# Optimization experiments

Hardware: AMD Instinct MI355X
Metric: run time of the kernel (lower is better)

The kernel has to match this reference:

```python
import jax, jax.numpy as jnp
import numpy as np

# ---- static config (Phi-3-small layer 0, blocksparse branch) ----
HIDDEN = 4096
N_HEADS = 32
N_KV = 8
HEAD_DIM = HIDDEN // N_HEADS        # 128
Q_PER_KV = N_HEADS // N_KV          # 4
SEQ = 2048
ROPE_BASE = 1000000.0
POS_SCALE = 1.0
SM_SCALE = 1.0 / HEAD_DIM           # mup scaling, multiplier=1.0
BLOCK = 64
LOCAL_BLOCKS = 16
VERT_STRIDE = 8


def _blocksparse_mask(seq_len):
    """Dense [S,S] bool mask realizing the causal blocksparse pattern:
    query block i attends key block j iff j<=i and (i-j < LOCAL_BLOCKS or (j+1) % VERT_STRIDE == 0),
    with elementwise causality inside blocks. Built once in numpy (static)."""
    nb = seq_len // BLOCK
    qb = np.arange(nb)[:, None]
    kb = np.arange(nb)[None, :]
    bmask = (kb <= qb) & ((qb - kb < LOCAL_BLOCKS) | ((kb + 1) % VERT_STRIDE == 0))
    emask = np.kron(bmask, np.ones((BLOCK, BLOCK), dtype=bool))
    i = np.arange(seq_len)
    emask &= i[:, None] >= i[None, :]
    return jnp.asarray(emask)


def _rope(x, cos, sin):
    # x: [B, S, H, D]; cos/sin: [S, D]
    x1, x2 = jnp.split(x, 2, axis=-1)
    rot = jnp.concatenate([-x2, x1], axis=-1)
    return x * cos[None, :, None, :] + rot * sin[None, :, None, :]


def setup_inputs() -> dict:
    key = jax.random.key(0)
    k1, k2, k3, k4, k5 = jax.random.split(key, 5)
    qkv_out = (N_HEADS + 2 * N_KV) * HEAD_DIM  # 6144
    return {
        "hidden_states": jax.random.normal(k1, (1, SEQ, HIDDEN), dtype=jnp.float32),
        "w_qkv": jax.random.normal(k2, (qkv_out, HIDDEN), dtype=jnp.float32) * 0.02,
        "b_qkv": jnp.zeros((qkv_out,), dtype=jnp.float32),
        "w_dense": jax.random.normal(k3, (HIDDEN, HIDDEN), dtype=jnp.float32) * 0.02,
        "b_dense": jnp.zeros((HIDDEN,), dtype=jnp.float32),
    }


def reference(hidden_states, w_qkv, b_qkv, w_dense, b_dense):
    B, S, _ = hidden_states.shape
    # grouped QKV projection: [B,S,(H+2*KV)*D]
    qkv = jnp.einsum("bsh,oh->bso", hidden_states, w_qkv) + b_qkv
    # group layout: (group, q0..q3, k, v) per kv head
    qkv = qkv.reshape(B, S, N_KV, Q_PER_KV + 2, HEAD_DIM)
    q = qkv[:, :, :, :Q_PER_KV].reshape(B, S, N_HEADS, HEAD_DIM)
    k = qkv[:, :, :, Q_PER_KV]   # [B,S,KV,D]
    v = qkv[:, :, :, Q_PER_KV + 1]
    # rotary embeddings (HF rotate-half style)
    inv_freq = 1.0 / (ROPE_BASE ** (jnp.arange(0, HEAD_DIM, 2, dtype=jnp.float32) / HEAD_DIM))
    t = jnp.arange(S, dtype=jnp.float32) * POS_SCALE
    freqs = jnp.outer(t, inv_freq)               # [S, D/2]
    emb = jnp.concatenate([freqs, freqs], axis=-1)
    cos, sin = jnp.cos(emb), jnp.sin(emb)
    q = _rope(q, cos, sin)
    k = _rope(k, cos, sin)
    # GQA: replicate kv heads to match q heads
    k = jnp.repeat(k, Q_PER_KV, axis=2)          # [B,S,H,D]
    v = jnp.repeat(v, Q_PER_KV, axis=2)
    mask = _blocksparse_mask(S)                  # [S,S] bool
    scores = jnp.einsum("bqhd,bkhd->bhqk", q, k) * SM_SCALE
    scores = jnp.where(mask[None, None], scores, jnp.finfo(scores.dtype).min)
    probs = jax.nn.softmax(scores, axis=-1)
    ctx = jnp.einsum("bhqk,bkhd->bqhd", probs, v).reshape(B, S, HIDDEN)
    out = jnp.einsum("bsh,oh->bso", ctx, w_dense) + b_dense
    return out
```

## Files before the change

kernel.cpp:

```cpp
#include <hip/hip_runtime.h>
#include <hip/hip_bf16.h>

#define SEQ 2048
#define HIDDEN 4096
#define NH 32
#define NKV 8
#define HD 128
#define QKV_OUT 6144
#define QSCALE (0.0078125f * 1.4426950408889634f)

typedef __attribute__((ext_vector_type(8))) short bf16x8;
typedef __attribute__((ext_vector_type(4))) float f32x4;
typedef __attribute__((ext_vector_type(16))) float f32x16;

__device__ inline unsigned short f32_bf16(float f) {
  union { float f; unsigned int u; } v; v.f = f;
  unsigned int r = v.u + 0x7FFFu + ((v.u >> 16) & 1u);
  return (unsigned short)(r >> 16);
}
__device__ inline float bf16_f32(unsigned short u) {
  union { unsigned int u; float f; } v; v.u = (unsigned int)u << 16;
  return v.f;
}
__device__ inline unsigned int pk(float a, float b) {
  union { __hip_bfloat162 h; unsigned int u; } t;
  t.h = __float22bfloat162_rn(make_float2(a, b));
  return t.u;
}
__device__ inline void pswap(unsigned int &a, unsigned int &b) {
  auto r = __builtin_amdgcn_permlane32_swap((int)a, (int)b, false, false);
  a = (unsigned int)r[0]; b = (unsigned int)r[1];
}
__device__ inline float xmax32(float v) {
  int x = __builtin_bit_cast(int, v);
  auto r = __builtin_amdgcn_permlane32_swap(x, x, false, false);
  return fmaxf(__builtin_bit_cast(float, (int)r[0]), __builtin_bit_cast(float, (int)r[1]));
}
__device__ inline float xadd32(float v) {
  int x = __builtin_bit_cast(int, v);
  auto r = __builtin_amdgcn_permlane32_swap(x, x, false, false);
  return __builtin_bit_cast(float, (int)r[0]) + __builtin_bit_cast(float, (int)r[1]);
}

__device__ inline void cast8(const float* __restrict__ in, unsigned short* __restrict__ out) {
  float4 a = *reinterpret_cast<const float4*>(in);
  float4 b = *reinterpret_cast<const float4*>(in + 4);
  unsigned short t[8];
  t[0] = f32_bf16(a.x); t[1] = f32_bf16(a.y); t[2] = f32_bf16(a.z); t[3] = f32_bf16(a.w);
  t[4] = f32_bf16(b.x); t[5] = f32_bf16(b.y); t[6] = f32_bf16(b.z); t[7] = f32_bf16(b.w);
  *reinterpret_cast<uint4*>(out) = *reinterpret_cast<uint4*>(t);
}

#define N1 ((size_t)SEQ * HIDDEN / 8)
#define N2 ((size_t)QKV_OUT * HIDDEN / 8)
#define N3 ((size_t)SEQ * 64)
__global__ __launch_bounds__(256) void prep(const float* __restrict__ hid,
                                            unsigned short* __restrict__ hid_bf,
                                            const float* __restrict__ wq,
                                            unsigned short* __restrict__ wq_bf,
                                            float* __restrict__ ct,
                                            float* __restrict__ st) {
  size_t i = (size_t)blockIdx.x * 256 + threadIdx.x;
  if (i < N1) {
    cast8(hid + i * 8, hid_bf + i * 8);
  } else if (i < N1 + N2) {
    size_t j = (i - N1) * 8;
    cast8(wq + j, wq_bf + j);
  } else {
    size_t j = i - N1 - N2;
    int s = (int)(j >> 6), d = (int)(j & 63);
    float inv = powf(1.0e6f, -(float)d * (1.0f / 64.0f));
    float f = (float)s * inv;
    ct[j] = cosf(f);
    st[j] = sinf(f);
  }
}

template <int BM, int CR, int CC, bool OBF, bool FC>
__global__ __launch_bounds__(512, 2) void gemm9(const unsigned short* __restrict__ A,
                                                const unsigned short* __restrict__ B,
                                                const float* __restrict__ bias,
                                                void* __restrict__ Cp,
                                                int M, int N, int K,
                                                const float* __restrict__ cw_in,
                                                unsigned short* __restrict__ cw_out,
                                                size_t cw_n, int ngemm) {
  constexpr int BN = 256;
  constexpr int MQ = BM / 64;
  constexpr int La = BM / 128;
  constexpr int Lb = 2;
  constexpr int AH = BM * 64;
  constexpr int BUF = AH * 2 + 32768;
  __shared__ __align__(16) char Lds[BUF * 2];

  if constexpr (FC) {
    if ((int)blockIdx.x >= ngemm) {
      size_t base = ((size_t)(blockIdx.x - ngemm) * 512 + threadIdx.x) * 8;
      size_t stride = (size_t)(gridDim.x - ngemm) * 512 * 8;
      for (size_t i = base; i < cw_n; i += stride)
        cast8(cw_in + i, cw_out + i);
      return;
    }
  }

  const int tid = threadIdx.x;
  const int wave = tid >> 6, lane = tid & 63;
  const int wr = wave >> 2, wc = wave & 3;
  const int lrow = lane & 15, lgrp = lane >> 4;

  const int ntx = N / BN;
  const int wg0 = blockIdx.x;
  const int xcd = wg0 & 7, w = wg0 >> 3;
  const int cpb = ntx / CC;
  const int band = xcd / cpb, colc = xcd % cpb;
  const int bm = (band * CR + w / CC) * BM;
  const int bn = (colc * CC + w % CC) * BN;

  const int srow8 = lane >> 3;
  const int scol = ((lane & 7) ^ srow8) * 8;
  const unsigned short* gsrc[2 * La + 2 * Lb];
  int ldsoff[2 * La + 2 * Lb];
#pragma unroll
  for (int u = 0; u < 2; ++u)
#pragma unroll
    for (int j = 0; j < La; ++j) {
      int row = bm + u * (BM / 2) + (wave * La + j) * 8 + srow8;
      gsrc[u * La + j] = A + (size_t)row * K + scol;
      ldsoff[u * La + j] = u * AH + (wave * La + j) * 1024;
    }
#pragma unroll
  for (int u = 0; u < 2; ++u)
#pragma unroll
    for (int j = 0; j < Lb; ++j) {
      int row = bn + u * 128 + (wave * Lb + j) * 8 + srow8;
      gsrc[2 * La + u * Lb + j] = B + (size_t)row * K + scol;
      ldsoff[2 * La + u * Lb + j] = 2 * AH + u * 16384 + (wave * Lb + j) * 1024;
    }

  auto stage = [&](int bufb, int u, int k0) {
    const int lo = (u < 2) ? u * La : 2 * La + (u - 2) * Lb;
    const int nl = (u < 2) ? La : Lb;
#pragma unroll
    for (int j = 0; j < 4; ++j)
      if (j < nl)
        __builtin_amdgcn_global_load_lds(
            (const __attribute__((address_space(1))) unsigned int*)(gsrc[lo + j] + k0),
            (__attribute__((address_space(3))) unsigned int*)(Lds + bufb + ldsoff[lo + j]),
            16, 0, 0);
  };

  const int rsw = (lrow & 7) << 4;
  auto aoff = [&](int mh, int m, int ks) {
    int r = mh * (BM / 4) + m * 16 + lrow;
    return wr * AH + r * 128 + ((ks * 64 + lgrp * 16) ^ rsw);
  };
  auto boff = [&](int nh, int n, int ks) {
    int r = (wc & 1) * 64 + nh * 32 + n * 16 + lrow;
    return 2 * AH + (wc >> 1) * 16384 + r * 128 + ((ks * 64 + lgrp * 16) ^ rsw);
  };

  f32x4 acc[2 * MQ][4] = {};
  bf16x8 af[MQ][2], bf0[2][2], bf1[2][2];

  const int nt = K / 64;
#pragma unroll
  for (int u = 0; u < 4; ++u) stage(0, u, 0);

  for (int t = 0; t < nt; ++t) {
    const int cur = (t & 1) ? BUF : 0;
    const int nxt = cur ^ BUF;
    const bool pf = (t + 1) < nt;
    const int k1 = (t + 1) * 64;
    const char* base = Lds + cur;

    if (pf) stage(nxt, 0, k1);
    if (pf) { if constexpr (La == 2) asm volatile("s_waitcnt vmcnt(2)" ::: "memory");
              else                   asm volatile("s_waitcnt vmcnt(1)" ::: "memory"); }
    else      asm volatile("s_waitcnt vmcnt(0)" ::: "memory");
    __builtin_amdgcn_sched_barrier(0);
    __builtin_amdgcn_s_barrier();
    __builtin_amdgcn_sched_barrier(0);
#pragma unroll
    for (int m = 0; m < MQ; ++m)
#pragma unroll
      for (int ks = 0; ks < 2; ++ks)
        af[m][ks] = *reinterpret_cast<const bf16x8*>(base + aoff(0, m, ks));
#pragma unroll
    for (int n = 0; n < 2; ++n)
#pragma unroll
      for (int ks = 0; ks < 2; ++ks)
        bf0[n][ks] = *reinterpret_cast<const bf16x8*>(base + boff(0, n, ks));
    __builtin_amdgcn_s_setprio(1);
#pragma unroll
    for (int m = 0; m < MQ; ++m)
#pragma unroll
      for (int n = 0; n < 2; ++n)
#pragma unroll
        for (int ks = 0; ks < 2; ++ks)
          acc[m][n] = __builtin_amdgcn_mfma_f32_16x16x32_bf16(af[m][ks], bf0[n][ks], acc[m][n], 0, 0, 0);
    __builtin_amdgcn_s_setprio(0);

    if (pf) stage(nxt, 1, k1);
#pragma unroll
    for (int n = 0; n < 2; ++n)
#pragma unroll
      for (int ks = 0; ks < 2; ++ks)
        bf1[n][ks] = *reinterpret_cast<const bf16x8*>(base + boff(1, n, ks));
    __builtin_amdgcn_s_setprio(1);
#pragma unroll
    for (int m = 0; m < MQ; ++m)
#pragma unroll
      for (int n = 0; n < 2; ++n)
#pragma unroll
        for (int ks = 0; ks < 2; ++ks)
          acc[m][2 + n] = __builtin_amdgcn_mfma_f32_16x16x32_bf16(af[m][ks], bf1[n][ks], acc[m][2 + n], 0, 0, 0);
    __builtin_amdgcn_s_setprio(0);

    if (pf) stage(nxt, 2, k1);
#pragma unroll
    for (int m = 0; m < MQ; ++m)
#pragma unroll
      for (int ks = 0; ks < 2; ++ks)
        af[m][ks] = *reinterpret_cast<const bf16x8*>(base + aoff(1, m, ks));
    __builtin_amdgcn_s_setprio(1);
#pragma unroll
    for (int m = 0; m < MQ; ++m)
#pragma unroll
      for (int n = 0; n < 2; ++n)
#pragma unroll
        for (int ks = 0; ks < 2; ++ks)
          acc[MQ + m][n] = __builtin_amdgcn_mfma_f32_16x16x32_bf16(af[m][ks], bf0[n][ks], acc[MQ + m][n], 0, 0, 0);
    __builtin_amdgcn_s_setprio(0);

    if (pf) stage(nxt, 3, k1);
    __builtin_amdgcn_s_setprio(1);
#pragma unroll
    for (int m = 0; m < MQ; ++m)
#pragma unroll
      for (int n = 0; n < 2; ++n)
#pragma unroll
        for (int ks = 0; ks < 2; ++ks)
          acc[MQ + m][2 + n] = __builtin_amdgcn_mfma_f32_16x16x32_bf16(af[m][ks], bf1[n][ks], acc[MQ + m][2 + n], 0, 0, 0);
    __builtin_amdgcn_s_setprio(0);
  }

#pragma unroll
  for (int ni = 0; ni < 4; ++ni) {
    int col = bn + wc * 64 + ni * 16 + lrow;
    float bv = bias[col];
#pragma unroll
    for (int mi = 0; mi < 2 * MQ; ++mi)
#pragma unroll
      for (int r = 0; r < 4; ++r) {
        int row = bm + wr * (BM / 2) + mi * 16 + lgrp * 4 + r;
        if constexpr (OBF)
          ((unsigned short*)Cp)[(size_t)row * N + col] = f32_bf16(acc[mi][ni][r] + bv);
        else
          ((float*)Cp)[(size_t)row * N + col] = acc[mi][ni][r] + bv;
      }
  }
}

__global__ __launch_bounds__(256) void rope_split(const unsigned short* __restrict__ qkvb,
                                                  const float* __restrict__ ct,
                                                  const float* __restrict__ st,
                                                  unsigned short* __restrict__ Q,
                                                  unsigned short* __restrict__ Kh,
                                                  unsigned short* __restrict__ Vt) {
  int b = blockIdx.x;
  if (b < 5120) {
    int t = b * 256 + threadIdx.x;
    int d8 = (t & 15) * 8;
    int q = t >> 4;
    int s = q / 40;
    int slotg = q - s * 40;
    int g = slotg / 5, slot = slotg - g * 5;
    const unsigned short* base = qkvb + (size_t)s * QKV_OUT + g * 768 + slot * 128;
    bf16x8 x8 = *reinterpret_cast<const bf16x8*>(base + d8);
    bf16x8 r8 = *reinterpret_cast<const bf16x8*>(base + (d8 ^ 64));
    float4 c0 = *reinterpret_cast<const float4*>(ct + s * 64 + (d8 & 63));
    float4 c1 = *reinterpret_cast<const float4*>(ct + s * 64 + (d8 & 63) + 4);
    float4 s0 = *reinterpret_cast<const float4*>(st + s * 64 + (d8 & 63));
    float4 s1 = *reinterpret_cast<const float4*>(st + s * 64 + (d8 & 63) + 4);
    float cc[8] = {c0.x, c0.y, c0.z, c0.w, c1.x, c1.y, c1.z, c1.w};
    float ss[8] = {s0.x, s0.y, s0.z, s0.w, s1.x, s1.y, s1.z, s1.w};
    float sgn = (d8 < 64) ? -1.0f : 1.0f;
    float sc = (slot < 4) ? QSCALE : 1.0f;
    unsigned short o[8];
#pragma unroll
    for (int i = 0; i < 8; ++i) {
      float x = bf16_f32((unsigned short)x8[i]);
      float r = bf16_f32((unsigned short)r8[i]) * sgn;
      o[i] = f32_bf16((x * cc[i] + r * ss[i]) * sc);
    }
    unsigned short* dst = (slot < 4)
        ? Q + ((size_t)(g * 4 + slot) * SEQ + s) * HD + d8
        : Kh + ((size_t)g * SEQ + s) * HD + d8;
    *reinterpret_cast<uint4*>(dst) = *reinterpret_cast<uint4*>(o);
  } else {
    int t2 = (b - 5120) * 256 + threadIdx.x;
    int d = t2 & 127;
    int rest = t2 >> 7;
    int g = rest & 7;
    int s0 = (rest >> 3) * 8;
    const unsigned short* src = qkvb + (size_t)s0 * QKV_OUT + g * 768 + 640 + d;
    unsigned short o[8];
#pragma unroll
    for (int i = 0; i < 8; ++i) o[i] = src[(size_t)i * QKV_OUT];
    *reinterpret_cast<uint4*>(&Vt[((size_t)g * HD + d) * SEQ + s0]) =
        *reinterpret_cast<uint4*>(o);
  }
}

__device__ inline int nextj(int x, int qb) {
  if (x > qb) return -1;
  if (qb - x < 16) return x;
  int v = (x & ~7) + 7;
  int w = qb - 15;
  return v < w ? v : w;
}

__global__ __launch_bounds__(256, 2) void attn32(const unsigned short* __restrict__ Q,
                                                 const unsigned short* __restrict__ Kh,
                                                 const unsigned short* __restrict__ Vt,
                                                 unsigned short* __restrict__ ctx) {
  const int g = blockIdx.x;
  const int y = (int)gridDim.y - 1 - (int)blockIdx.y;
  const int qb = y >> 1, half = y & 1;
  const int Q0 = y * 32;
  const int tid = threadIdx.x;
  const int wave = tid >> 6;
  const int h = g * 4 + wave;
  const int lane = tid & 63;
  const int l31 = lane & 31, hi = lane >> 5;

  __shared__ __align__(16) char Lds[65536];

  auto stage = [&](int bufb, int j) {
#pragma unroll
    for (int i = 0; i < 4; ++i) {
      int row = i * 16 + (tid >> 4);
      const unsigned short* src =
          Kh + ((size_t)(g * SEQ + j * 64 + row)) * HD + ((tid & 15) ^ (row & 15)) * 8;
      __builtin_amdgcn_global_load_lds(
          (const __attribute__((address_space(1))) unsigned int*)src,
          (__attribute__((address_space(3))) unsigned int*)(Lds + bufb + i * 4096 + (tid >> 6) * 1024),
          16, 0, 0);
    }
#pragma unroll
    for (int i = 0; i < 4; ++i) {
      int row = i * 32 + (tid >> 3);
      const unsigned short* src =
          Vt + ((size_t)(g * HD + row)) * SEQ + j * 64 + ((tid & 7) ^ (row & 7)) * 8;
      __builtin_amdgcn_global_load_lds(
          (const __attribute__((address_space(1))) unsigned int*)src,
          (__attribute__((address_space(3))) unsigned int*)(Lds + bufb + 16384 + i * 4096 + (tid >> 6) * 1024),
          16, 0, 0);
    }
  };

  bf16x8 qf[8];
  const unsigned short* qbase = Q + ((size_t)h * SEQ + Q0 + l31) * HD;
#pragma unroll
  for (int kk = 0; kk < 8; ++kk)
    qf[kk] = *reinterpret_cast<const bf16x8*>(qbase + kk * 16 + hi * 8);

  f32x16 ot[4] = {};
  float mrow = -1e30f, lsum = 0.f;

  const int kswz = l31 & 15;
  const int vswz = l31 & 7;

  int j = nextj(0, qb);
  int cur = 0;
  stage(0, j);
  asm volatile("s_waitcnt vmcnt(0)" ::: "memory");
  __builtin_amdgcn_sched_barrier(0);
  __builtin_amdgcn_s_barrier();
  __builtin_amdgcn_sched_barrier(0);

  while (true) {
    const int jn = (j < qb) ? nextj(j + 1, qb) : -1;
    if (jn >= 0) stage(cur ^ 32768, jn);

    const char* kb = Lds + cur;
    const char* vb = Lds + cur + 16384;
    const bool diag = (j == qb);
    const bool short_blk = diag && (half == 0);

    f32x16 st[2] = {};
    __builtin_amdgcn_s_setprio(1);
#pragma unroll
    for (int kk = 0; kk < 8; ++kk) {
      bf16x8 k0 = *reinterpret_cast<const bf16x8*>(
          kb + (size_t)l31 * 256 + (((2 * kk + hi) ^ kswz) * 16));
      st[0] = __builtin_amdgcn_mfma_f32_32x32x16_bf16(k0, qf[kk], st[0], 0, 0, 0);
      if (!short_blk) {
        bf16x8 k1 = *reinterpret_cast<const bf16x8*>(
            kb + (size_t)(32 + l31) * 256 + (((2 * kk + hi) ^ kswz) * 16));
        st[1] = __builtin_amdgcn_mfma_f32_32x32x16_bf16(k1, qf[kk], st[1], 0, 0, 0);
      }
    }
    __builtin_amdgcn_s_setprio(0);

    if (diag) {
      int qrel = half * 32 + l31;
#pragma unroll
      for (int kt = 0; kt < 2; ++kt)
#pragma unroll
        for (int r = 0; r < 16; ++r) {
          int krel = kt * 32 + (r & 3) + 8 * (r >> 2) + 4 * hi;
          if (krel > qrel) st[kt][r] = -1e30f;
        }
    }

    float t16[16];
#pragma unroll
    for (int r = 0; r < 16; ++r) t16[r] = fmaxf(st[0][r], st[1][r]);
#pragma unroll
    for (int sft = 8; sft >= 1; sft >>= 1)
#pragma unroll
      for (int r = 0; r < sft; ++r) t16[r] = fmaxf(t16[r], t16[r + sft]);
    float vm = xmax32(t16[0]);

    if (!__all(vm - mrow <= 8.0f)) {
      float nm = fmaxf(mrow, vm);
      float corr = __builtin_amdgcn_exp2f(mrow - nm);
      lsum *= corr;
#pragma unroll
      for (int dt = 0; dt < 4; ++dt)
#pragma unroll
        for (int r = 0; r < 16; ++r) ot[dt][r] *= corr;
      mrow = nm;
    }

    float s4[4] = {0.f, 0.f, 0.f, 0.f};
#pragma unroll
    for (int kt = 0; kt < 2; ++kt)
#pragma unroll
      for (int r = 0; r < 16; ++r) {
        float p = __builtin_amdgcn_exp2f(st[kt][r] - mrow);
        st[kt][r] = p;
        s4[r & 3] += p;
      }
    lsum += xadd32((s4[0] + s4[1]) + (s4[2] + s4[3]));

    bf16x8 pb[4];
#pragma unroll
    for (int s = 0; s < 4; ++s) {
      int kt = s >> 1, g0 = (s & 1) * 2, g1 = g0 + 1;
      unsigned int a0 = pk(st[kt][4 * g0 + 0], st[kt][4 * g0 + 1]);
      unsigned int a1 = pk(st[kt][4 * g0 + 2], st[kt][4 * g0 + 3]);
      unsigned int b0 = pk(st[kt][4 * g1 + 0], st[kt][4 * g1 + 1]);
      unsigned int b1 = pk(st[kt][4 * g1 + 2], st[kt][4 * g1 + 3]);
      pswap(a0, b0);
      pswap(a1, b1);
      union { unsigned int u[4]; bf16x8 v; } t;
      t.u[0] = a0; t.u[1] = a1; t.u[2] = b0; t.u[3] = b1;
      pb[s] = t.v;
    }

    const int smax = short_blk ? 2 : 4;
    __builtin_amdgcn_s_setprio(1);
#pragma unroll
    for (int dt = 0; dt < 4; ++dt) {
      const char* vrow = vb + (size_t)(dt * 32 + l31) * 128;
#pragma unroll
      for (int s = 0; s < 4; ++s)
        if (s < smax)
          ot[dt] = __builtin_amdgcn_mfma_f32_32x32x16_bf16(
              *reinterpret_cast<const bf16x8*>(vrow + (((2 * s + hi) ^ vswz) * 16)),
              pb[s], ot[dt], 0, 0, 0);
    }
    __builtin_amdgcn_s_setprio(0);

    if (jn < 0) break;
    asm volatile("s_waitcnt vmcnt(0)" ::: "memory");
    __builtin_amdgcn_sched_barrier(0);
    __builtin_amdgcn_s_barrier();
    __builtin_amdgcn_sched_barrier(0);
    j = jn;
    cur ^= 32768;
  }

  __syncthreads();
  char* W = Lds + wave * 8192;
  float inv = 1.0f / lsum;
  const int swz = (l31 & 7) << 4;
#pragma unroll
  for (int dt = 0; dt < 4; ++dt)
#pragma unroll
    for (int gg = 0; gg < 4; ++gg) {
      unsigned int u0 = pk(ot[dt][4 * gg + 0] * inv, ot[dt][4 * gg + 1] * inv);
      unsigned int u1 = pk(ot[dt][4 * gg + 2] * inv, ot[dt][4 * gg + 3] * inv);
      int off = (dt * 64 + gg * 16 + hi * 8) ^ swz;
      *reinterpret_cast<uint2*>(W + l31 * 256 + off) = make_uint2(u0, u1);
    }
#pragma unroll
  for (int i = 0; i < 8; ++i) {
    int row = lane >> 1;
    int t = (lane & 1) * 8 + i;
    bf16x8 vv = *reinterpret_cast<const bf16x8*>(
        W + row * 256 + ((t * 16) ^ ((row & 7) << 4)));
    *reinterpret_cast<bf16x8*>(&ctx[(size_t)(Q0 + row) * HIDDEN + h * HD + t * 8]) = vv;
  }
}

extern "C" void kernel_launch(void* const* d_in, const int* in_sizes, int n_in,
                              void* d_out, int out_size, void* d_ws, size_t ws_size,
                              hipStream_t stream) {
  const float* hidden  = (const float*)d_in[0];
  const float* w_qkv   = (const float*)d_in[1];
  const float* b_qkv   = (const float*)d_in[2];
  const float* w_dense = (const float*)d_in[3];
  const float* b_dense = (const float*)d_in[4];
  float* out = (float*)d_out;

  char* p = (char*)d_ws;
  unsigned short* hid_bf  = (unsigned short*)p; p += (size_t)SEQ * HIDDEN * 2;
  unsigned short* wqkv_bf = (unsigned short*)p; p += (size_t)QKV_OUT * HIDDEN * 2;
  unsigned short* wd_bf   = (unsigned short*)p; p += (size_t)HIDDEN * HIDDEN * 2;
  unsigned short* qkvb    = (unsigned short*)p; p += (size_t)SEQ * QKV_OUT * 2;
  unsigned short* Qb      = (unsigned short*)p; p += (size_t)NH * SEQ * HD * 2;
  unsigned short* Kb      = (unsigned short*)p; p += (size_t)NKV * SEQ * HD * 2;
  unsigned short* Vt      = (unsigned short*)p; p += (size_t)NKV * HD * SEQ * 2;
  float* ct               = (float*)p;          p += (size_t)SEQ * 64 * 4;
  float* st               = (float*)p;          p += (size_t)SEQ * 64 * 4;
  unsigned short* ctx = hid_bf;

  const int prep_blocks = (int)((N1 + N2 + N3 + 255) / 256);
  prep<<<prep_blocks, 256, 0, stream>>>(hidden, hid_bf, w_qkv, wqkv_bf, ct, st);

  const int ngemm_qkv = (SEQ / 128) * (QKV_OUT / 256);
  gemm9<128, 8, 6, true, true>
      <<<dim3(ngemm_qkv + 192), 512, 0, stream>>>(
          hid_bf, wqkv_bf, b_qkv, qkvb, SEQ, QKV_OUT, HIDDEN,
          w_dense, wd_bf, (size_t)HIDDEN * HIDDEN, ngemm_qkv);
  rope_split<<<5120 + 1024, 256, 0, stream>>>(qkvb, ct, st, Qb, Kb, Vt);
  attn32<<<dim3(NKV, SEQ / 32), 256, 0, stream>>>(Qb, Kb, Vt, ctx);
  gemm9<128, 8, 4, false, false>
      <<<dim3((SEQ / 128) * (HIDDEN / 256)), 512, 0, stream>>>(
          ctx, wd_bf, b_dense, out, SEQ, HIDDEN, HIDDEN,
          nullptr, nullptr, 0, 0);
}
```

Before: 299.4 us.

## Generalize GEMM tile width, use 256x192 QKV tiles, move dense-weight cast into prep

The GEMM template now takes a configurable BN, with B staging and fragment loops generalized. The QKV projection switches to 256x192 tiles, giving a grid of 256 blocks instead of 384 plus 192 cast blocks. The w_dense fp32-to-bf16 cast moves out of the GEMM's extra blocks and into the prep kernel. The aim is better operand reuse and a single wave of blocks for the QKV GEMM, at the cost of more LDS and registers per block and a longer, serialized prep kernel.

```diff
diff --git a/kernel.cpp b/kernel.cpp
--- a/kernel.cpp
+++ b/kernel.cpp
@@ -53,11 +53,14 @@
 
 #define N1 ((size_t)SEQ * HIDDEN / 8)
 #define N2 ((size_t)QKV_OUT * HIDDEN / 8)
+#define N4 ((size_t)HIDDEN * HIDDEN / 8)
 #define N3 ((size_t)SEQ * 64)
 __global__ __launch_bounds__(256) void prep(const float* __restrict__ hid,
                                             unsigned short* __restrict__ hid_bf,
                                             const float* __restrict__ wq,
                                             unsigned short* __restrict__ wq_bf,
+                                            const float* __restrict__ wd,
+                                            unsigned short* __restrict__ wd_bf,
                                             float* __restrict__ ct,
                                             float* __restrict__ st) {
   size_t i = (size_t)blockIdx.x * 256 + threadIdx.x;
@@ -66,8 +69,11 @@
   } else if (i < N1 + N2) {
     size_t j = (i - N1) * 8;
     cast8(wq + j, wq_bf + j);
+  } else if (i < N1 + N2 + N4) {
+    size_t j = (i - N1 - N2) * 8;
+    cast8(wd + j, wd_bf + j);
   } else {
-    size_t j = i - N1 - N2;
+    size_t j = i - N1 - N2 - N4;
     int s = (int)(j >> 6), d = (int)(j & 63);
     float inv = powf(1.0e6f, -(float)d * (1.0f / 64.0f));
     float f = (float)s * inv;
@@ -76,32 +82,21 @@
   }
 }
 
-template <int BM, int CR, int CC, bool OBF, bool FC>
-__global__ __launch_bounds__(512, 2) void gemm9(const unsigned short* __restrict__ A,
+template <int BM, int BN, int CR, int CC, bool OBF>
+__global__ __launch_bounds__(512, 2) void gemmG(const unsigned short* __restrict__ A,
                                                 const unsigned short* __restrict__ B,
                                                 const float* __restrict__ bias,
                                                 void* __restrict__ Cp,
-                                                int M, int N, int K,
-                                                const float* __restrict__ cw_in,
-                                                unsigned short* __restrict__ cw_out,
-                                                size_t cw_n, int ngemm) {
-  constexpr int BN = 256;
-  constexpr int MQ = BM / 64;
-  constexpr int La = BM / 128;
-  constexpr int Lb = 2;
-  constexpr int AH = BM * 64;
-  constexpr int BUF = AH * 2 + 32768;
-  __shared__ __align__(16) char Lds[BUF * 2];
-
-  if constexpr (FC) {
-    if ((int)blockIdx.x >= ngemm) {
-      size_t base = ((size_t)(blockIdx.x - ngemm) * 512 + threadIdx.x) * 8;
-      size_t stride = (size_t)(gridDim.x - ngemm) * 512 * 8;
-      for (size_t i = base; i < cw_n; i += stride)
-        cast8(cw_in + i, cw_out + i);
-      return;
-    }
-  }
+                                                int M, int N, int K) {
+  constexpr int MQ   = BM / 64;
+  constexpr int NREP = BN / 64;
+  constexpr int NB0  = (NREP + 1) / 2;
+  constexpr int La   = BM / 128;
+  constexpr int NB   = BN / 64;
+  constexpr int NBQ2 = (NB + 1) / 2;
+  constexpr int AH   = BM * 64;
+  constexpr int SB   = 2 * AH + BN * 128;
+  __shared__ __align__(16) char Lds[SB * 2];
 
   const int tid = threadIdx.x;
   const int wave = tid >> 6, lane = tid & 63;
@@ -116,37 +111,40 @@
   const int bm = (band * CR + w / CC) * BM;
   const int bn = (colc * CC + w % CC) * BN;
 
-  const int srow8 = lane >> 3;
-  const int scol = ((lane & 7) ^ srow8) * 8;
-  const unsigned short* gsrc[2 * La + 2 * Lb];
-  int ldsoff[2 * La + 2 * Lb];
+  const int r8 = lane >> 3;
+  const int scol = ((lane & 7) ^ r8) * 8;
+
+  const unsigned short* gA[2][La]; int lA[2][La];
 #pragma unroll
   for (int u = 0; u < 2; ++u)
 #pragma unroll
     for (int j = 0; j < La; ++j) {
-      int row = bm + u * (BM / 2) + (wave * La + j) * 8 + srow8;
-      gsrc[u * La + j] = A + (size_t)row * K + scol;
-      ldsoff[u * La + j] = u * AH + (wave * La + j) * 1024;
-    }
-#pragma unroll
-  for (int u = 0; u < 2; ++u)
-#pragma unroll
-    for (int j = 0; j < Lb; ++j) {
-      int row = bn + u * 128 + (wave * Lb + j) * 8 + srow8;
-      gsrc[2 * La + u * Lb + j] = B + (size_t)row * K + scol;
-      ldsoff[2 * La + u * Lb + j] = 2 * AH + u * 16384 + (wave * Lb + j) * 1024;
-    }
-
-  auto stage = [&](int bufb, int u, int k0) {
-    const int lo = (u < 2) ? u * La : 2 * La + (u - 2) * Lb;
-    const int nl = (u < 2) ? La : Lb;
-#pragma unroll
-    for (int j = 0; j < 4; ++j)
-      if (j < nl)
+      int row = bm + u * (BM / 2) + wave * (BM / 16) + j * 8 + r8;
+      gA[u][j] = A + (size_t)row * K + scol;
+      lA[u][j] = u * AH + (wave * (BM / 16) + j * 8) * 128;
+    }
+  const unsigned short* gB[NB]; int lB[NB];
+#pragma unroll
+  for (int j = 0; j < NB; ++j) {
+    int row = bn + wave * (BN / 8) + j * 8 + r8;
+    gB[j] = B + (size_t)row * K + scol;
+    lB[j] = 2 * AH + (wave * (BN / 8) + j * 8) * 128;
+  }
+
+  auto stageA = [&](int bufb, int u, int k0) {
+#pragma unroll
+    for (int j = 0; j < La; ++j)
+      __builtin_amdgcn_global_load_lds(
+          (const __attribute__((address_space(1))) unsigned int*)(gA[u][j] + k0),
+          (__attribute__((address_space(3))) unsigned int*)(Lds + bufb + lA[u][j]), 16, 0, 0);
+  };
+  auto stageB = [&](int bufb, int jlo, int jhi, int k0) {
+#pragma unroll
+    for (int j = 0; j < NB; ++j)
+      if (j >= jlo && j < jhi)
         __builtin_amdgcn_global_load_lds(
-            (const __attribute__((address_space(1))) unsigned int*)(gsrc[lo + j] + k0),
-            (__attribute__((address_space(3))) unsigned int*)(Lds + bufb + ldsoff[lo + j]),
-            16, 0, 0);
+            (const __attribute__((address_space(1))) unsigned int*)(gB[j] + k0),
+            (__attribute__((address_space(3))) unsigned int*)(Lds + bufb + lB[j]), 16, 0, 0);
   };
 
   const int rsw = (lrow & 7) << 4;
@@ -154,26 +152,27 @@
     int r = mh * (BM / 4) + m * 16 + lrow;
     return wr * AH + r * 128 + ((ks * 64 + lgrp * 16) ^ rsw);
   };
-  auto boff = [&](int nh, int n, int ks) {
-    int r = (wc & 1) * 64 + nh * 32 + n * 16 + lrow;
-    return 2 * AH + (wc >> 1) * 16384 + r * 128 + ((ks * 64 + lgrp * 16) ^ rsw);
+  auto boff = [&](int nf, int ks) {
+    int r = wc * (BN / 4) + nf * 16 + lrow;
+    return 2 * AH + r * 128 + ((ks * 64 + lgrp * 16) ^ rsw);
   };
 
-  f32x4 acc[2 * MQ][4] = {};
-  bf16x8 af[MQ][2], bf0[2][2], bf1[2][2];
+  f32x4 acc[2 * MQ][NREP] = {};
+  bf16x8 af[MQ][2], bf[NREP][2];
 
   const int nt = K / 64;
-#pragma unroll
-  for (int u = 0; u < 4; ++u) stage(0, u, 0);
+  stageA(0, 0, 0);
+  stageA(0, 1, 0);
+  stageB(0, 0, NB, 0);
 
   for (int t = 0; t < nt; ++t) {
-    const int cur = (t & 1) ? BUF : 0;
-    const int nxt = cur ^ BUF;
+    const int cur = (t & 1) ? SB : 0;
+    const int nxt = cur ^ SB;
     const bool pf = (t + 1) < nt;
     const int k1 = (t + 1) * 64;
     const char* base = Lds + cur;
 
-    if (pf) stage(nxt, 0, k1);
+    if (pf) stageA(nxt, 0, k1);
     if (pf) { if constexpr (La == 2) asm volatile("s_waitcnt vmcnt(2)" ::: "memory");
               else                   asm volatile("s_waitcnt vmcnt(1)" ::: "memory"); }
     else      asm volatile("s_waitcnt vmcnt(0)" ::: "memory");
@@ -186,37 +185,37 @@
       for (int ks = 0; ks < 2; ++ks)
         af[m][ks] = *reinterpret_cast<const bf16x8*>(base + aoff(0, m, ks));
 #pragma unroll
-    for (int n = 0; n < 2; ++n)
+    for (int nf = 0; nf < NB0; ++nf)
 #pragma unroll
       for (int ks = 0; ks < 2; ++ks)
-        bf0[n][ks] = *reinterpret_cast<const bf16x8*>(base + boff(0, n, ks));
+        bf[nf][ks] = *reinterpret_cast<const bf16x8*>(base + boff(nf, ks));
     __builtin_amdgcn_s_setprio(1);
 #pragma unroll
     for (int m = 0; m < MQ; ++m)
 #pragma unroll
-      for (int n = 0; n < 2; ++n)
+      for (int nf = 0; nf < NB0; ++nf)
 #pragma unroll
         for (int ks = 0; ks < 2; ++ks)
-          acc[m][n] = __builtin_amdgcn_mfma_f32_16x16x32_bf16(af[m][ks], bf0[n][ks], acc[m][n], 0, 0, 0);
+          acc[m][nf] = __builtin_amdgcn_mfma_f32_16x16x32_bf16(af[m][ks], bf[nf][ks], acc[m][nf], 0, 0, 0);
     __builtin_amdgcn_s_setprio(0);
 
-    if (pf) stage(nxt, 1, k1);
-#pragma unroll
-    for (int n = 0; n < 2; ++n)
+    if (pf) stageA(nxt, 1, k1);
+#pragma unroll
+    for (int nf = NB0; nf < NREP; ++nf)
 #pragma unroll
       for (int ks = 0; ks < 2; ++ks)
-        bf1[n][ks] = *reinterpret_cast<const bf16x8*>(base + boff(1, n, ks));
+        bf[nf][ks] = *reinterpret_cast<const bf16x8*>(base + boff(nf, ks));
     __builtin_amdgcn_s_setprio(1);
 #pragma unroll
     for (int m = 0; m < MQ; ++m)
 #pragma unroll
-      for (int n = 0; n < 2; ++n)
+      for (int nf = NB0; nf < NREP; ++nf)
 #pragma unroll
         for (int ks = 0; ks < 2; ++ks)
-          acc[m][2 + n] = __builtin_amdgcn_mfma_f32_16x16x32_bf16(af[m][ks], bf1[n][ks], acc[m][2 + n], 0, 0, 0);
+          acc[m][nf] = __builtin_amdgcn_mfma_f32_16x16x32_bf16(af[m][ks], bf[nf][ks], acc[m][nf], 0, 0, 0);
     __builtin_amdgcn_s_setprio(0);
 
-    if (pf) stage(nxt, 2, k1);
+    if (pf) stageB(nxt, 0, NBQ2, k1);
 #pragma unroll
     for (int m = 0; m < MQ; ++m)
 #pragma unroll
@@ -226,27 +225,27 @@
 #pragma unroll
     for (int m = 0; m < MQ; ++m)
 #pragma unroll
-      for (int n = 0; n < 2; ++n)
+      for (int nf = 0; nf < NB0; ++nf)
 #pragma unroll
         for (int ks = 0; ks < 2; ++ks)
-          acc[MQ + m][n] = __builtin_amdgcn_mfma_f32_16x16x32_bf16(af[m][ks], bf0[n][ks], acc[MQ + m][n], 0, 0, 0);
+          acc[MQ + m][nf] = __builtin_amdgcn_mfma_f32_16x16x32_bf16(af[m][ks], bf[nf][ks], acc[MQ + m][nf], 0, 0, 0);
     __builtin_amdgcn_s_setprio(0);
 
-    if (pf) stage(nxt, 3, k1);
+    if (pf) stageB(nxt, NBQ2, NB, k1);
     __builtin_amdgcn_s_setprio(1);
 #pragma unroll
     for (int m = 0; m < MQ; ++m)
 #pragma unroll
-      for (int n = 0; n < 2; ++n)
+      for (int nf = NB0; nf < NREP; ++nf)
 #pragma unroll
         for (int ks = 0; ks < 2; ++ks)
-          acc[MQ + m][2 + n] = __builtin_amdgcn_mfma_f32_16x16x32_bf16(af[m][ks], bf1[n][ks], acc[MQ + m][2 + n], 0, 0, 0);
+          acc[MQ + m][nf] = __builtin_amdgcn_mfma_f32_16x16x32_bf16(af[m][ks], bf[nf][ks], acc[MQ + m][nf], 0, 0, 0);
     __builtin_amdgcn_s_setprio(0);
   }
 
 #pragma unroll
-  for (int ni = 0; ni < 4; ++ni) {
-    int col = bn + wc * 64 + ni * 16 + lrow;
+  for (int ni = 0; ni < NREP; ++ni) {
+    int col = bn + wc * (BN / 4) + ni * 16 + lrow;
     float bv = bias[col];
 #pragma unroll
     for (int mi = 0; mi < 2 * MQ; ++mi)
@@ -528,18 +527,16 @@
   float* st               = (float*)p;          p += (size_t)SEQ * 64 * 4;
   unsigned short* ctx = hid_bf;
 
-  const int prep_blocks = (int)((N1 + N2 + N3 + 255) / 256);
-  prep<<<prep_blocks, 256, 0, stream>>>(hidden, hid_bf, w_qkv, wqkv_bf, ct, st);
-
-  const int ngemm_qkv = (SEQ / 128) * (QKV_OUT / 256);
-  gemm9<128, 8, 6, true, true>
-      <<<dim3(ngemm_qkv + 192), 512, 0, stream>>>(
-          hid_bf, wqkv_bf, b_qkv, qkvb, SEQ, QKV_OUT, HIDDEN,
-          w_dense, wd_bf, (size_t)HIDDEN * HIDDEN, ngemm_qkv);
+  const int prep_blocks = (int)((N1 + N2 + N4 + N3 + 255) / 256);
+  prep<<<prep_blocks, 256, 0, stream>>>(hidden, hid_bf, w_qkv, wqkv_bf,
+                                        w_dense, wd_bf, ct, st);
+
+  gemmG<256, 192, 4, 8, true>
+      <<<dim3((SEQ / 256) * (QKV_OUT / 192)), 512, 0, stream>>>(
+          hid_bf, wqkv_bf, b_qkv, qkvb, SEQ, QKV_OUT, HIDDEN);
   rope_split<<<5120 + 1024, 256, 0, stream>>>(qkvb, ct, st, Qb, Kb, Vt);
   attn32<<<dim3(NKV, SEQ / 32), 256, 0, stream>>>(Qb, Kb, Vt, ctx);
-  gemm9<128, 8, 4, false, false>
+  gemmG<128, 256, 8, 4, false>
       <<<dim3((SEQ / 128) * (HIDDEN / 256)), 512, 0, stream>>>(
-          ctx, wd_bf, b_dense, out, SEQ, HIDDEN, HIDDEN,
-          nullptr, nullptr, 0, 0);
-}
+          ctx, wd_bf, b_dense, out, SEQ, HIDDEN, HIDDEN);
+}
```

Result: faster. 274.7 us (-8.3%).
